# Performance work log

Hardware: AMD Instinct MI355X
Metric: run time of the kernel (lower is better)

The kernel has to match this reference:

```python
import jax, jax.numpy as jnp
import numpy as np


def _dct2(x):
    """DCT-II over last dim, scipy norm=None scaling (matches the torch rfft trick:
    X_k = 2 * sum_n x_n cos(pi*k*(2n+1)/(2N))). Expressed as one batched matmul."""
    N = x.shape[-1]
    n = jnp.arange(N, dtype=x.dtype)
    k = jnp.arange(N, dtype=x.dtype)
    # D[k, n] = 2*cos(pi*k*(2n+1)/(2N))
    D = 2.0 * jnp.cos((np.pi / (2.0 * N)) * k[:, None] * (2.0 * n[None, :] + 1.0))
    return jnp.einsum('kn,bcn->bck', D, x)


def setup_inputs() -> dict:
    key = jax.random.key(0)
    k0, k1, k2 = jax.random.split(key, 3)
    b, c, l = 32, 512, 1024
    x = jax.random.normal(k0, (b, c, l), dtype=jnp.float32)
    # 1x1 Conv1d weights (kernel_size=1, bias=False) stored as [out, in]
    w1 = jax.random.normal(k1, (2 * c, c), dtype=jnp.float32) / np.float32(np.sqrt(c))
    w2 = jax.random.normal(k2, (c, 2 * c), dtype=jnp.float32) / np.float32(np.sqrt(2 * c))
    ln_w = jnp.ones((l,), dtype=jnp.float32)
    ln_b = jnp.zeros((l,), dtype=jnp.float32)
    return {"x": x, "w1": w1, "w2": w2, "ln_w": ln_w, "ln_b": ln_b}


def reference(x, w1, w2, ln_w, ln_b):
    eps = 1e-6
    freq = _dct2(x)                                   # [b, c, l]
    mu = jnp.mean(freq, axis=-1, keepdims=True)
    var = jnp.var(freq, axis=-1, keepdims=True)       # biased, like nn.LayerNorm
    h = (freq - mu) * jax.lax.rsqrt(var + eps) * ln_w + ln_b
    # fc: Conv1d(c->2c, k=1) -> Dropout(eval: identity) -> ReLU -> Conv1d(2c->c) -> Sigmoid
    h = jax.nn.relu(jnp.einsum('oi,bil->bol', w1, h))  # [b, 2c, l]
    gate = jax.nn.sigmoid(jnp.einsum('oi,bil->bol', w2, h))  # [b, c, l]
    return x * gate
```

## Files before the change

### kernel.cpp

```cpp
#include <hip/hip_runtime.h>
#include <hip/hip_bf16.h>
#include <math.h>

typedef short short8 __attribute__((ext_vector_type(8)));
typedef short short4v __attribute__((ext_vector_type(4)));
typedef float f32x4 __attribute__((ext_vector_type(4)));

__device__ __forceinline__ short f2bf(float f) {
  union { float f; unsigned u; } v; v.f = f;
  unsigned r = v.u + 0x7FFFu + ((v.u >> 16) & 1u);
  return (short)(r >> 16);
}
__device__ __forceinline__ float bf2f(short s) {
  union { unsigned u; float f; } v; v.u = ((unsigned)(unsigned short)s) << 16;
  return v.f;
}

__global__ __launch_bounds__(256) void cast_kernel(const float* __restrict__ in,
                                                   short* __restrict__ out, int n4) {
  int i = blockIdx.x * blockDim.x + threadIdx.x;
  if (i < n4) {
    float4 v = ((const float4*)in)[i];
    short4v o;
    o.x = f2bf(v.x); o.y = f2bf(v.y); o.z = f2bf(v.z); o.w = f2bf(v.w);
    ((short4v*)out)[i] = o;
  }
}

__global__ __launch_bounds__(256) void build_D(short* __restrict__ D) {
  int t = blockIdx.x * 256 + threadIdx.x;
  int k = t >> 10, n = t & 1023;
  const float s = 1.5339807878856412e-03f;
  float arg = (s * (float)k) * (float)(2 * n + 1);
  D[t] = f2bf(2.0f * cosf(arg));
}

__global__ __launch_bounds__(256) void ln_stats(const float2* __restrict__ partial,
                                                float2* __restrict__ musd) {
  int n = blockIdx.x * 256 + threadIdx.x;
  float S = 0.f, Q = 0.f;
#pragma unroll
  for (int r = 0; r < 4; ++r) {
    float2 p = partial[(size_t)r * 16384 + n];
    S += p.x; Q += p.y;
  }
  float mu  = S * (1.f / 1024.f);
  float var = Q * (1.f / 1024.f) - mu * mu;
  float2 o; o.x = mu; o.y = rsqrtf(var + 1e-6f);
  musd[n] = o;
}

__global__ __launch_bounds__(256) void ln_apply(short* __restrict__ freqT,
                                                const float2* __restrict__ musd,
                                                const float* __restrict__ lnw,
                                                const float* __restrict__ lnb) {
  int t = blockIdx.x * 256 + threadIdx.x;
  int c8 = t & 63;
  int k  = (t >> 6) & 1023;
  int b  = t >> 16;
  size_t idx = ((size_t)b << 19) + (size_t)k * 512 + (size_t)c8 * 8;
  short8 v = *(const short8*)&freqT[idx];
  float w  = lnw[k];
  float bb = lnb[k];
  const float2* ms = &musd[b * 512 + c8 * 8];
  short8 o;
#pragma unroll
  for (int j = 0; j < 8; ++j) {
    float f = bf2f(v[j]);
    float2 m = ms[j];
    o[j] = f2bf((f - m.x) * m.y * w + bb);
  }
  *(short8*)&freqT[idx] = o;
}

template<int EPI>
__global__ __launch_bounds__(512, 2) void gemm256(
    const short* __restrict__ A, const short* __restrict__ B,
    void* __restrict__ Cout, const float* __restrict__ X,
    float2* __restrict__ P, int K, int NT, long strideA, long strideB)
{
  __shared__ short As[2][16384];
  __shared__ short Bs[2][16384];
  const int tid = threadIdx.x;
  const int l   = tid & 63;
  const int w   = tid >> 6;
  const int wm  = w >> 2;
  const int wn  = w & 3;
  const int l7  = l & 7;
  const int lr  = l & 15;
  const int lhi = l >> 4;

  const int nwg = gridDim.x, q = nwg >> 3, orig = blockIdx.x;
  const int wgid = (orig & 7) * q + (orig >> 3);
  int bx, by, bz;
  if (EPI == 0)      { bx = wgid & 3; by = wgid >> 2;      bz = 0; }
  else if (EPI == 1) { bx = wgid & 3; by = (wgid >> 2) & 3; bz = wgid >> 4; }
  else               { by = wgid & 3; bx = (wgid >> 2) & 1; bz = wgid >> 3; }

  const long row0 = (long)bx * 256, col0 = (long)by * 256;
  const short* Ab = A + (size_t)bz * strideA + (size_t)row0 * K;
  const short* Bb = B + (size_t)bz * strideB + (size_t)col0 * K;

  const int rowb  = w * 8 + (l >> 3);
  const int colel = (l7 ^ (l >> 3)) * 8;
  const int arow = (wm * 128 + lr) * 64;
  const int brow = (wn * 64  + lr) * 64;
  const int sk0 = ((lhi    ) ^ l7) * 8;
  const int sk1 = ((lhi + 4) ^ l7) * 8;

  f32x4 acc[8][4];
#pragma unroll
  for (int i = 0; i < 8; ++i)
#pragma unroll
    for (int j = 0; j < 4; ++j) acc[i][j] = (f32x4){0.f, 0.f, 0.f, 0.f};

#define STAGE(KT, D) do {                                                    \
    const size_t ko_ = (size_t)(KT) * 64 + colel;                            \
    _Pragma("unroll")                                                        \
    for (int r_ = 0; r_ < 4; ++r_)                                           \
      __builtin_amdgcn_global_load_lds(                                      \
        (const __attribute__((address_space(1))) void*)(Ab + (size_t)(r_*64 + rowb)*K + ko_), \
        (__attribute__((address_space(3))) void*)(&As[D][r_*4096 + w*512 + l*8]), 16, 0, 0);  \
    _Pragma("unroll")                                                        \
    for (int r_ = 0; r_ < 4; ++r_)                                           \
      __builtin_amdgcn_global_load_lds(                                      \
        (const __attribute__((address_space(1))) void*)(Bb + (size_t)(r_*64 + rowb)*K + ko_), \
        (__attribute__((address_space(3))) void*)(&Bs[D][r_*4096 + w*512 + l*8]), 16, 0, 0);  \
  } while (0)

  STAGE(0, 0);
  STAGE(1, 1);

  short8 b0, b1, b2, b3;
  int cur = 0;
  for (int kt = 0; kt < NT; ++kt) {
    if (kt + 1 < NT) { asm volatile("s_waitcnt vmcnt(8)" ::: "memory"); }
    else             { asm volatile("s_waitcnt vmcnt(0)" ::: "memory"); }
    __builtin_amdgcn_sched_barrier(0);
    __builtin_amdgcn_s_barrier();
    const short* Ad = As[cur];
    const short* Bd = Bs[cur];
    short8 a0, a1, a2, a3;

#define MFMA_ROW(MI, AV)                                                       \
    acc[MI][0] = __builtin_amdgcn_mfma_f32_16x16x32_bf16(AV, b0, acc[MI][0], 0, 0, 0); \
    acc[MI][1] = __builtin_amdgcn_mfma_f32_16x16x32_bf16(AV, b1, acc[MI][1], 0, 0, 0); \
    acc[MI][2] = __builtin_amdgcn_mfma_f32_16x16x32_bf16(AV, b2, acc[MI][2], 0, 0, 0); \
    acc[MI][3] = __builtin_amdgcn_mfma_f32_16x16x32_bf16(AV, b3, acc[MI][3], 0, 0, 0);

#define PH(MIBASE, SK, LOADB)                                                \
    a0 = *(const short8*)&Ad[arow + (MIBASE + 0) * 1024 + SK];               \
    a1 = *(const short8*)&Ad[arow + (MIBASE + 1) * 1024 + SK];               \
    a2 = *(const short8*)&Ad[arow + (MIBASE + 2) * 1024 + SK];               \
    a3 = *(const short8*)&Ad[arow + (MIBASE + 3) * 1024 + SK];               \
    if (LOADB) {                                                             \
      b0 = *(const short8*)&Bd[brow + 0 * 1024 + SK];                        \
      b1 = *(const short8*)&Bd[brow + 1 * 1024 + SK];                        \
      b2 = *(const short8*)&Bd[brow + 2 * 1024 + SK];                        \
      b3 = *(const short8*)&Bd[brow + 3 * 1024 + SK];                        \
    }                                                                        \
    __builtin_amdgcn_s_barrier();                                            \
    asm volatile("s_waitcnt lgkmcnt(0)" ::: "memory");                       \
    __builtin_amdgcn_sched_barrier(0);                                       \
    __builtin_amdgcn_s_setprio(1);                                           \
    MFMA_ROW(MIBASE + 0, a0); MFMA_ROW(MIBASE + 1, a1);                      \
    MFMA_ROW(MIBASE + 2, a2); MFMA_ROW(MIBASE + 3, a3);                      \
    __builtin_amdgcn_s_setprio(0);                                           \
    __builtin_amdgcn_sched_barrier(0);                                       \
    __builtin_amdgcn_s_barrier();

    PH(0, sk0, 1)
    PH(4, sk0, 0)
    PH(0, sk1, 1)
    PH(4, sk1, 0)

    if (kt + 2 < NT) STAGE(kt + 2, cur);
    cur ^= 1;
  }

  const int rb = (int)row0 + wm * 128 + lhi * 4;
  const int cb = (int)col0 + wn * 64 + lr;
  float sv[4], qv[4];
#pragma unroll
  for (int ni = 0; ni < 4; ++ni) { sv[ni] = 0.f; qv[ni] = 0.f; }

#pragma unroll
  for (int mi = 0; mi < 8; ++mi) {
#pragma unroll
    for (int ni = 0; ni < 4; ++ni) {
#pragma unroll
      for (int j = 0; j < 4; ++j) {
        int r  = rb + mi * 16 + j;
        int cc = cb + ni * 16;
        float v = acc[mi][ni][j];
        if (EPI == 0) {
          sv[ni] += v; qv[ni] += v * v;
          ((short*)Cout)[((size_t)(cc >> 9) << 19) + (size_t)r * 512 + (cc & 511)] = f2bf(v);
        } else if (EPI == 1) {
          ((short*)Cout)[(size_t)bz * 1048576 + (size_t)r * 1024 + cc] = f2bf(v > 0.f ? v : 0.f);
        } else {
          size_t idx = (size_t)bz * 524288 + (size_t)r * 1024 + cc;
          float g = 1.f / (1.f + __expf(-v));
          ((float*)Cout)[idx] = X[idx] * g;
        }
      }
    }
  }

  if (EPI == 0) {
    __syncthreads();
    float* redS = (float*)&As[0][0];
    float* redQ = redS + 2048;
    const int contrib = wm * 4 + lhi;
#pragma unroll
    for (int ni = 0; ni < 4; ++ni) {
      int ccl = wn * 64 + ni * 16 + lr;
      redS[ccl * 8 + contrib] = sv[ni];
      redQ[ccl * 8 + contrib] = qv[ni];
    }
    __syncthreads();
    if (tid < 256) {
      float S = 0.f, Q = 0.f;
#pragma unroll
      for (int i = 0; i < 8; ++i) { S += redS[tid * 8 + i]; Q += redQ[tid * 8 + i]; }
      float2 o; o.x = S; o.y = Q;
      P[(size_t)bx * 16384 + col0 + tid] = o;
    }
  }
#undef PH
#undef MFMA_ROW
#undef STAGE
}

extern "C" void kernel_launch(void* const* d_in, const int* in_sizes, int n_in,
                              void* d_out, int out_size, void* d_ws, size_t ws_size,
                              hipStream_t stream) {
  const float* x    = (const float*)d_in[0];
  const float* w1   = (const float*)d_in[1];
  const float* w2   = (const float*)d_in[2];
  const float* ln_w = (const float*)d_in[3];
  const float* ln_b = (const float*)d_in[4];
  float* out = (float*)d_out;

  char* ws = (char*)d_ws;
  short* x_bf   = (short*)(ws);
  short* D_bf   = (short*)(ws + 33554432);
  short* w1_bf  = (short*)(ws + 35651584);
  short* w2_bf  = (short*)(ws + 36700160);
  short* freqT  = (short*)(ws + 37748736);
  short* z1t    = (short*)(ws + 71303168);
  float2* part  = (float2*)(ws + 138412032);
  float2* musd  = (float2*)(ws + 139460608);

  cast_kernel<<<dim3(16384), dim3(256), 0, stream>>>(x,  x_bf,  16777216 / 4);
  cast_kernel<<<dim3(512),   dim3(256), 0, stream>>>(w1, w1_bf, 524288 / 4);
  cast_kernel<<<dim3(512),   dim3(256), 0, stream>>>(w2, w2_bf, 524288 / 4);
  build_D<<<dim3(4096), dim3(256), 0, stream>>>(D_bf);

  gemm256<0><<<dim3(256), dim3(512), 0, stream>>>(
      D_bf, x_bf, (void*)freqT, nullptr, part, 1024, 16, 0, 0);

  ln_stats<<<dim3(64), dim3(256), 0, stream>>>(part, musd);

  ln_apply<<<dim3(8192), dim3(256), 0, stream>>>(freqT, musd, ln_w, ln_b);

  gemm256<1><<<dim3(512), dim3(512), 0, stream>>>(
      freqT, w1_bf, (void*)z1t, nullptr, nullptr, 512, 8, 524288, 0);

  gemm256<2><<<dim3(256), dim3(512), 0, stream>>>(
      w2_bf, z1t, (void*)out, x, nullptr, 1024, 16, 0, 1048576);
}
```

Measured before the change: 193.0 us.

## Split DCT into even/odd half-size GEMMs and switch to 128x128 tiles

New measurement: 160.5 us. 16.8% less time.

```diff
diff --git a/kernel.cpp b/kernel.cpp
--- a/kernel.cpp
+++ b/kernel.cpp
@@ -27,11 +27,26 @@
   }
 }
 
-__global__ __launch_bounds__(256) void build_D(short* __restrict__ D) {
+__global__ __launch_bounds__(256) void prep_eo(const float* __restrict__ x,
+                                               short* __restrict__ eo) {
   int t = blockIdx.x * 256 + threadIdx.x;
-  int k = t >> 10, n = t & 1023;
+  int bc = t >> 7, n0 = (t & 127) * 4;
+  const float* xr = x + (size_t)bc * 1024;
+  float4 f = *(const float4*)(xr + n0);
+  float4 r = *(const float4*)(xr + 1020 - n0);
+  short4v ef, of;
+  ef.x = f2bf(f.x + r.w); ef.y = f2bf(f.y + r.z); ef.z = f2bf(f.z + r.y); ef.w = f2bf(f.w + r.x);
+  of.x = f2bf(f.x - r.w); of.y = f2bf(f.y - r.z); of.z = f2bf(f.z - r.y); of.w = f2bf(f.w - r.x);
+  *(short4v*)&eo[(size_t)bc * 512 + n0] = ef;
+  *(short4v*)&eo[8388608 + (size_t)bc * 512 + n0] = of;
+}
+
+__global__ __launch_bounds__(256) void build_Deo(short* __restrict__ D) {
+  int t = blockIdx.x * 256 + threadIdx.x;
+  int parity = t >> 18, rem = t & 262143;
+  int k2 = rem >> 9, n = rem & 511;
   const float s = 1.5339807878856412e-03f;
-  float arg = (s * (float)k) * (float)(2 * n + 1);
+  float arg = (s * (float)(2 * k2 + parity)) * (float)(2 * n + 1);
   D[t] = f2bf(2.0f * cosf(arg));
 }
 
@@ -40,7 +55,7 @@
   int n = blockIdx.x * 256 + threadIdx.x;
   float S = 0.f, Q = 0.f;
 #pragma unroll
-  for (int r = 0; r < 4; ++r) {
+  for (int r = 0; r < 8; ++r) {
     float2 p = partial[(size_t)r * 16384 + n];
     S += p.x; Q += p.y;
   }
@@ -74,18 +89,18 @@
 }
 
 template<int EPI>
-__global__ __launch_bounds__(512, 2) void gemm256(
+__global__ __launch_bounds__(256, 2) void gemm128(
     const short* __restrict__ A, const short* __restrict__ B,
     void* __restrict__ Cout, const float* __restrict__ X,
     float2* __restrict__ P, int K, int NT, long strideA, long strideB)
 {
-  __shared__ short As[2][16384];
-  __shared__ short Bs[2][16384];
+  __shared__ short As[2][8192];
+  __shared__ short Bs[2][8192];
   const int tid = threadIdx.x;
   const int l   = tid & 63;
   const int w   = tid >> 6;
-  const int wm  = w >> 2;
-  const int wn  = w & 3;
+  const int wm  = w >> 1;
+  const int wc  = w & 1;
   const int l7  = l & 7;
   const int lr  = l & 15;
   const int lhi = l >> 4;
@@ -93,109 +108,119 @@
   const int nwg = gridDim.x, q = nwg >> 3, orig = blockIdx.x;
   const int wgid = (orig & 7) * q + (orig >> 3);
   int bx, by, bz;
-  if (EPI == 0)      { bx = wgid & 3; by = wgid >> 2;      bz = 0; }
-  else if (EPI == 1) { bx = wgid & 3; by = (wgid >> 2) & 3; bz = wgid >> 4; }
-  else               { by = wgid & 3; bx = (wgid >> 2) & 1; bz = wgid >> 3; }
-
-  const long row0 = (long)bx * 256, col0 = (long)by * 256;
+  if (EPI == 0)      { bx = wgid & 3; bz = (wgid >> 2) & 1; by = wgid >> 3; }
+  else if (EPI == 1) { by = wgid & 7; bx = (wgid >> 3) & 7; bz = wgid >> 6; }
+  else               { bx = wgid & 3; by = (wgid >> 2) & 7; bz = wgid >> 5; }
+
+  const long row0 = (long)bx * 128, col0 = (long)by * 128;
   const short* Ab = A + (size_t)bz * strideA + (size_t)row0 * K;
   const short* Bb = B + (size_t)bz * strideB + (size_t)col0 * K;
 
-  const int rowb  = w * 8 + (l >> 3);
-  const int colel = (l7 ^ (l >> 3)) * 8;
-  const int arow = (wm * 128 + lr) * 64;
-  const int brow = (wn * 64  + lr) * 64;
-  const int sk0 = ((lhi    ) ^ l7) * 8;
-  const int sk1 = ((lhi + 4) ^ l7) * 8;
-
-  f32x4 acc[8][4];
-#pragma unroll
-  for (int i = 0; i < 8; ++i)
+  const int rowb  = tid >> 3;
+  const int colel = ((tid & 7) ^ ((tid >> 3) & 7)) * 8;
+  const int abase = (wm * 64 + lr) * 64;
+  const int bbase = (wc * 64 + lr) * 64;
+  const int s0 = ((lhi    ) ^ l7) * 8;
+  const int s1 = ((lhi + 4) ^ l7) * 8;
+
+  f32x4 acc[4][4];
+#pragma unroll
+  for (int i = 0; i < 4; ++i)
 #pragma unroll
     for (int j = 0; j < 4; ++j) acc[i][j] = (f32x4){0.f, 0.f, 0.f, 0.f};
+
+#define GLL(SRC, DST) __builtin_amdgcn_global_load_lds(                      \
+      (const __attribute__((address_space(1))) void*)(SRC),                  \
+      (__attribute__((address_space(3))) void*)(DST), 16, 0, 0)
 
 #define STAGE(KT, D) do {                                                    \
     const size_t ko_ = (size_t)(KT) * 64 + colel;                            \
     _Pragma("unroll")                                                        \
     for (int r_ = 0; r_ < 4; ++r_)                                           \
-      __builtin_amdgcn_global_load_lds(                                      \
-        (const __attribute__((address_space(1))) void*)(Ab + (size_t)(r_*64 + rowb)*K + ko_), \
-        (__attribute__((address_space(3))) void*)(&As[D][r_*4096 + w*512 + l*8]), 16, 0, 0);  \
+      GLL(Ab + (size_t)(r_ * 32 + rowb) * K + ko_,                           \
+          &As[D][(r_ * 32 + rowb) * 64 + (tid & 7) * 8]);                    \
     _Pragma("unroll")                                                        \
     for (int r_ = 0; r_ < 4; ++r_)                                           \
-      __builtin_amdgcn_global_load_lds(                                      \
-        (const __attribute__((address_space(1))) void*)(Bb + (size_t)(r_*64 + rowb)*K + ko_), \
-        (__attribute__((address_space(3))) void*)(&Bs[D][r_*4096 + w*512 + l*8]), 16, 0, 0);  \
+      GLL(Bb + (size_t)(r_ * 32 + rowb) * K + ko_,                           \
+          &Bs[D][(r_ * 32 + rowb) * 64 + (tid & 7) * 8]);                    \
   } while (0)
+
+#define LD8(PTR, OFF) (*(const short8*)&(PTR)[OFF])
+#define MFMA(AV, BV, C) __builtin_amdgcn_mfma_f32_16x16x32_bf16(AV, BV, C, 0, 0, 0)
+#define SBAR __builtin_amdgcn_s_barrier()
+#define SCHB __builtin_amdgcn_sched_barrier(0)
+
+#define MFMA16(A0, A1, A2, A3, B0, B1, B2, B3)                               \
+    __builtin_amdgcn_s_setprio(1);                                           \
+    acc[0][0]=MFMA(A0,B0,acc[0][0]); acc[0][1]=MFMA(A0,B1,acc[0][1]);        \
+    acc[0][2]=MFMA(A0,B2,acc[0][2]); acc[0][3]=MFMA(A0,B3,acc[0][3]);        \
+    acc[1][0]=MFMA(A1,B0,acc[1][0]); acc[1][1]=MFMA(A1,B1,acc[1][1]);        \
+    acc[1][2]=MFMA(A1,B2,acc[1][2]); acc[1][3]=MFMA(A1,B3,acc[1][3]);        \
+    acc[2][0]=MFMA(A2,B0,acc[2][0]); acc[2][1]=MFMA(A2,B1,acc[2][1]);        \
+    acc[2][2]=MFMA(A2,B2,acc[2][2]); acc[2][3]=MFMA(A2,B3,acc[2][3]);        \
+    acc[3][0]=MFMA(A3,B0,acc[3][0]); acc[3][1]=MFMA(A3,B1,acc[3][1]);        \
+    acc[3][2]=MFMA(A3,B2,acc[3][2]); acc[3][3]=MFMA(A3,B3,acc[3][3]);        \
+    __builtin_amdgcn_s_setprio(0);
 
   STAGE(0, 0);
   STAGE(1, 1);
 
-  short8 b0, b1, b2, b3;
   int cur = 0;
   for (int kt = 0; kt < NT; ++kt) {
     if (kt + 1 < NT) { asm volatile("s_waitcnt vmcnt(8)" ::: "memory"); }
     else             { asm volatile("s_waitcnt vmcnt(0)" ::: "memory"); }
-    __builtin_amdgcn_sched_barrier(0);
-    __builtin_amdgcn_s_barrier();
+    SCHB; SBAR;
     const short* Ad = As[cur];
     const short* Bd = Bs[cur];
-    short8 a0, a1, a2, a3;
-
-#define MFMA_ROW(MI, AV)                                                       \
-    acc[MI][0] = __builtin_amdgcn_mfma_f32_16x16x32_bf16(AV, b0, acc[MI][0], 0, 0, 0); \
-    acc[MI][1] = __builtin_amdgcn_mfma_f32_16x16x32_bf16(AV, b1, acc[MI][1], 0, 0, 0); \
-    acc[MI][2] = __builtin_amdgcn_mfma_f32_16x16x32_bf16(AV, b2, acc[MI][2], 0, 0, 0); \
-    acc[MI][3] = __builtin_amdgcn_mfma_f32_16x16x32_bf16(AV, b3, acc[MI][3], 0, 0, 0);
-
-#define PH(MIBASE, SK, LOADB)                                                \
-    a0 = *(const short8*)&Ad[arow + (MIBASE + 0) * 1024 + SK];               \
-    a1 = *(const short8*)&Ad[arow + (MIBASE + 1) * 1024 + SK];               \
-    a2 = *(const short8*)&Ad[arow + (MIBASE + 2) * 1024 + SK];               \
-    a3 = *(const short8*)&Ad[arow + (MIBASE + 3) * 1024 + SK];               \
-    if (LOADB) {                                                             \
-      b0 = *(const short8*)&Bd[brow + 0 * 1024 + SK];                        \
-      b1 = *(const short8*)&Bd[brow + 1 * 1024 + SK];                        \
-      b2 = *(const short8*)&Bd[brow + 2 * 1024 + SK];                        \
-      b3 = *(const short8*)&Bd[brow + 3 * 1024 + SK];                        \
-    }                                                                        \
-    __builtin_amdgcn_s_barrier();                                            \
-    asm volatile("s_waitcnt lgkmcnt(0)" ::: "memory");                       \
-    __builtin_amdgcn_sched_barrier(0);                                       \
-    __builtin_amdgcn_s_setprio(1);                                           \
-    MFMA_ROW(MIBASE + 0, a0); MFMA_ROW(MIBASE + 1, a1);                      \
-    MFMA_ROW(MIBASE + 2, a2); MFMA_ROW(MIBASE + 3, a3);                      \
-    __builtin_amdgcn_s_setprio(0);                                           \
-    __builtin_amdgcn_sched_barrier(0);                                       \
-    __builtin_amdgcn_s_barrier();
-
-    PH(0, sk0, 1)
-    PH(4, sk0, 0)
-    PH(0, sk1, 1)
-    PH(4, sk1, 0)
-
+    short8 a00, a01, a02, a03, b00, b01, b02, b03;
+    short8 a10, a11, a12, a13, b10, b11, b12, b13;
+    a00 = LD8(Ad, abase + 0 * 1024 + s0);
+    a01 = LD8(Ad, abase + 1 * 1024 + s0);
+    a02 = LD8(Ad, abase + 2 * 1024 + s0);
+    a03 = LD8(Ad, abase + 3 * 1024 + s0);
+    b00 = LD8(Bd, bbase + 0 * 1024 + s0);
+    b01 = LD8(Bd, bbase + 1 * 1024 + s0);
+    b02 = LD8(Bd, bbase + 2 * 1024 + s0);
+    b03 = LD8(Bd, bbase + 3 * 1024 + s0);
+    a10 = LD8(Ad, abase + 0 * 1024 + s1);
+    a11 = LD8(Ad, abase + 1 * 1024 + s1);
+    a12 = LD8(Ad, abase + 2 * 1024 + s1);
+    a13 = LD8(Ad, abase + 3 * 1024 + s1);
+    b10 = LD8(Bd, bbase + 0 * 1024 + s1);
+    b11 = LD8(Bd, bbase + 1 * 1024 + s1);
+    b12 = LD8(Bd, bbase + 2 * 1024 + s1);
+    b13 = LD8(Bd, bbase + 3 * 1024 + s1);
+    SCHB;
+    asm volatile("s_waitcnt lgkmcnt(8)" ::: "memory");
+    SCHB;
+    MFMA16(a00, a01, a02, a03, b00, b01, b02, b03)
+    SCHB;
+    asm volatile("s_waitcnt lgkmcnt(0)" ::: "memory");
+    SCHB; SBAR;
     if (kt + 2 < NT) STAGE(kt + 2, cur);
+    SCHB;
+    MFMA16(a10, a11, a12, a13, b10, b11, b12, b13)
+    SCHB;
     cur ^= 1;
   }
 
-  const int rb = (int)row0 + wm * 128 + lhi * 4;
-  const int cb = (int)col0 + wn * 64 + lr;
   float sv[4], qv[4];
 #pragma unroll
   for (int ni = 0; ni < 4; ++ni) { sv[ni] = 0.f; qv[ni] = 0.f; }
 
 #pragma unroll
-  for (int mi = 0; mi < 8; ++mi) {
+  for (int mi = 0; mi < 4; ++mi) {
 #pragma unroll
     for (int ni = 0; ni < 4; ++ni) {
 #pragma unroll
       for (int j = 0; j < 4; ++j) {
-        int r  = rb + mi * 16 + j;
-        int cc = cb + ni * 16;
+        int r  = (int)row0 + wm * 64 + mi * 16 + lhi * 4 + j;
+        int cc = (int)col0 + wc * 64 + ni * 16 + lr;
         float v = acc[mi][ni][j];
         if (EPI == 0) {
           sv[ni] += v; qv[ni] += v * v;
-          ((short*)Cout)[((size_t)(cc >> 9) << 19) + (size_t)r * 512 + (cc & 511)] = f2bf(v);
+          int rr = r * 2 + bz;
+          ((short*)Cout)[((size_t)(cc >> 9) << 19) + (size_t)rr * 512 + (cc & 511)] = f2bf(v);
         } else if (EPI == 1) {
           ((short*)Cout)[(size_t)bz * 1048576 + (size_t)r * 1024 + cc] = f2bf(v > 0.f ? v : 0.f);
         } else {
@@ -210,26 +235,30 @@
   if (EPI == 0) {
     __syncthreads();
     float* redS = (float*)&As[0][0];
-    float* redQ = redS + 2048;
+    float* redQ = redS + 1024;
     const int contrib = wm * 4 + lhi;
 #pragma unroll
     for (int ni = 0; ni < 4; ++ni) {
-      int ccl = wn * 64 + ni * 16 + lr;
+      int ccl = wc * 64 + ni * 16 + lr;
       redS[ccl * 8 + contrib] = sv[ni];
       redQ[ccl * 8 + contrib] = qv[ni];
     }
     __syncthreads();
-    if (tid < 256) {
+    if (tid < 128) {
       float S = 0.f, Q = 0.f;
 #pragma unroll
       for (int i = 0; i < 8; ++i) { S += redS[tid * 8 + i]; Q += redQ[tid * 8 + i]; }
       float2 o; o.x = S; o.y = Q;
-      P[(size_t)bx * 16384 + col0 + tid] = o;
+      P[(size_t)(bz * 4 + bx) * 16384 + col0 + tid] = o;
     }
   }
-#undef PH
-#undef MFMA_ROW
+#undef MFMA16
+#undef MFMA
+#undef LD8
 #undef STAGE
+#undef GLL
+#undef SBAR
+#undef SCHB
 }
 
 extern "C" void kernel_launch(void* const* d_in, const int* in_sizes, int n_in,
@@ -243,30 +272,30 @@
   float* out = (float*)d_out;
 
   char* ws = (char*)d_ws;
-  short* x_bf   = (short*)(ws);
-  short* D_bf   = (short*)(ws + 33554432);
-  short* w1_bf  = (short*)(ws + 35651584);
-  short* w2_bf  = (short*)(ws + 36700160);
-  short* freqT  = (short*)(ws + 37748736);
-  short* z1t    = (short*)(ws + 71303168);
-  float2* part  = (float2*)(ws + 138412032);
-  float2* musd  = (float2*)(ws + 139460608);
-
-  cast_kernel<<<dim3(16384), dim3(256), 0, stream>>>(x,  x_bf,  16777216 / 4);
-  cast_kernel<<<dim3(512),   dim3(256), 0, stream>>>(w1, w1_bf, 524288 / 4);
-  cast_kernel<<<dim3(512),   dim3(256), 0, stream>>>(w2, w2_bf, 524288 / 4);
-  build_D<<<dim3(4096), dim3(256), 0, stream>>>(D_bf);
-
-  gemm256<0><<<dim3(256), dim3(512), 0, stream>>>(
-      D_bf, x_bf, (void*)freqT, nullptr, part, 1024, 16, 0, 0);
+  short* Deo    = (short*)(ws);
+  short* w1_bf  = (short*)(ws + 1048576);
+  short* w2_bf  = (short*)(ws + 2097152);
+  short* freqT  = (short*)(ws + 3145728);
+  short* z1t    = (short*)(ws + 36700160);
+  short* eo     = z1t;
+  float2* part  = (float2*)(ws + 103809024);
+  float2* musd  = (float2*)(ws + 104857600);
+
+  prep_eo<<<dim3(8192), dim3(256), 0, stream>>>(x, eo);
+  cast_kernel<<<dim3(512), dim3(256), 0, stream>>>(w1, w1_bf, 524288 / 4);
+  cast_kernel<<<dim3(512), dim3(256), 0, stream>>>(w2, w2_bf, 524288 / 4);
+  build_Deo<<<dim3(2048), dim3(256), 0, stream>>>(Deo);
+
+  gemm128<0><<<dim3(1024), dim3(256), 0, stream>>>(
+      Deo, eo, (void*)freqT, nullptr, part, 512, 8, 262144, 8388608);
 
   ln_stats<<<dim3(64), dim3(256), 0, stream>>>(part, musd);
 
   ln_apply<<<dim3(8192), dim3(256), 0, stream>>>(freqT, musd, ln_w, ln_b);
 
-  gemm256<1><<<dim3(512), dim3(512), 0, stream>>>(
+  gemm128<1><<<dim3(2048), dim3(256), 0, stream>>>(
       freqT, w1_bf, (void*)z1t, nullptr, nullptr, 512, 8, 524288, 0);
 
-  gemm256<2><<<dim3(256), dim3(512), 0, stream>>>(
+  gemm128<2><<<dim3(1024), dim3(256), 0, stream>>>(
       w2_bf, z1t, (void*)out, x, nullptr, 1024, 16, 0, 1048576);
 }
```
